# Optimization experiments

Measured on AMD Instinct MI355X. Metric: run time of the kernel, lower is better.

The kernel has to match this reference:

```python
import jax, jax.numpy as jnp
import numpy as np

B, L, H, E, D = 2, 2048, 8, 64, 64


def setup_inputs() -> dict:
    key = jax.random.key(0)
    k0, k1, k2, k3 = jax.random.split(key, 4)
    u = jax.random.normal(k0, (B, L, H, D), dtype=jnp.float32)
    q = jax.random.normal(k1, (B, L, H, E), dtype=jnp.float32)
    k = jax.random.normal(k2, (B, L, H, E), dtype=jnp.float32)
    v = jax.random.normal(k3, (B, L, H, D), dtype=jnp.float32)
    # causal mask: True where attention is DISALLOWED (strict upper triangle)
    attn_mask = jnp.triu(jnp.ones((L, L), dtype=bool), k=1)[None, None]  # (1,1,L,L)
    return {"u": u, "q": q, "k": k, "v": v, "attn_mask": attn_mask}


def reference(u, q, k, v, attn_mask):
    # q,k: [B,L,H,E]; v,u: [B,L,H,D]; attn_mask: [1,1,L,S] bool (True = masked)
    Edim = q.shape[-1]
    S = k.shape[1]
    scale = 1.0 / np.sqrt(Edim)
    scores = jnp.einsum('blhe,bshe->bhls', q, k)  # [B,H,L,S]
    x = jax.nn.relu(scale * scores)
    # attention_normalize(method='squared_relu'): relu(x)^2 / seq_len; masked -> 0
    A = jnp.where(attn_mask, 0.0, x * x) / S  # [B,H,L,S]
    # dropout is identity in eval mode
    V = u * jnp.einsum('bhls,bshd->blhd', A, v)  # [B,L,H,D]
    return V
```

## Files before the change

kernel.cpp:

```cpp
#include <hip/hip_runtime.h>
#include <hip/hip_bf16.h>

namespace {
constexpr int Lc = 2048, Hc = 8;
constexpr int RS = Hc * 64;
constexpr int NKT = 32;
constexpr int TILE_BYTES = 16384;
}

typedef __attribute__((ext_vector_type(8))) short bf16x8;
typedef __attribute__((ext_vector_type(16))) float f32x16;
typedef unsigned int u32;
typedef __attribute__((ext_vector_type(4))) u32 u32x4;

__device__ __forceinline__ u32 bfu(float x) {
    return (u32)__builtin_bit_cast(unsigned short, __float2bfloat16(x));
}
__device__ __forceinline__ short f2bf(float x) {
    return (short)__builtin_bit_cast(unsigned short, __float2bfloat16(x));
}

#define MFMA32(a, b, c) __builtin_amdgcn_mfma_f32_32x32x16_bf16((a), (b), (c), 0, 0, 0)

#define GLL16(gp, lp) __builtin_amdgcn_global_load_lds( \
    (const __attribute__((address_space(1))) unsigned int*)(gp), \
    (__attribute__((address_space(3))) unsigned int*)(lp), 16, 0, 0)

__global__ __launch_bounds__(256)
void prep_kv(const float* __restrict__ kg, const float* __restrict__ vg,
             short* __restrict__ ws)
{
    const int kt = blockIdx.x, bh = blockIdx.y;
    const int b = bh >> 3, h = bh & 7;
    const size_t base = ((size_t)b * Lc * Hc + h) * 64;
    char* tile = (char*)ws + (size_t)(bh * NKT + kt) * TILE_BYTES;
    const int tid = threadIdx.x;

    {
        const int c = tid & 7, e0 = c * 8;
        #pragma unroll
        for (int p = 0; p < 2; ++p) {
            const int s = (tid >> 3) + 32 * p;
            const float* src = kg + base + (size_t)(kt * 64 + s) * RS + e0;
            float4 x0 = *(const float4*)src;
            float4 x1 = *(const float4*)(src + 4);
            bf16x8 w = { f2bf(x0.x), f2bf(x0.y), f2bf(x0.z), f2bf(x0.w),
                         f2bf(x1.x), f2bf(x1.y), f2bf(x1.z), f2bf(x1.w) };
            const int lane = (c & 1) * 32 + (s & 31);
            const int byte = ((s >> 5) * 4 + (c >> 1)) * 1024 + lane * 16;
            *(bf16x8*)(tile + byte) = w;
        }
    }
    {
        const int d = tid & 63;
        #pragma unroll
        for (int p = 0; p < 2; ++p) {
            const int sblk = (tid >> 6) + 4 * p;
            const int s0 = sblk * 8;
            float xv[8];
            #pragma unroll
            for (int j = 0; j < 8; ++j)
                xv[j] = vg[base + (size_t)(kt * 64 + s0 + j) * RS + d];
            bf16x8 w = { f2bf(xv[0]), f2bf(xv[1]), f2bf(xv[2]), f2bf(xv[3]),
                         f2bf(xv[4]), f2bf(xv[5]), f2bf(xv[6]), f2bf(xv[7]) };
            const int lane = (sblk & 1) * 32 + (d & 31);
            const int byte = 8192 + ((d >> 5) * 4 + (sblk >> 1)) * 1024 + lane * 16;
            *(bf16x8*)(tile + byte) = w;
        }
    }
}

__global__ __launch_bounds__(512, 1)
void gate_attn(const float* __restrict__ ug, const float* __restrict__ qg,
               const short* __restrict__ ws, float* __restrict__ outg)
{
    __shared__ __align__(16) char lds[2][4 * TILE_BYTES];

    const int tid = threadIdx.x;
    const int wave = tid >> 6, lane = tid & 63;
    const int col = lane & 31, hi = lane >> 5;
    const int qs = wave & 1, ktp = wave >> 1;

    const int pr = blockIdx.x, bh = blockIdx.y;
    const int b = bh >> 3, h = bh & 7;
    const size_t base = ((size_t)b * Lc * Hc + h) * 64;
    const char* wsbh = (const char*)ws + (size_t)bh * NKT * TILE_BYTES;

    auto STAGEG = [&](int t0, int buf) {
        const char* src = wsbh + (size_t)t0 * TILE_BYTES + tid * 16;
        char* dst = &lds[buf][0] + tid * 16;
        #pragma unroll
        for (int i = 0; i < 8; ++i)
            GLL16(src + i * 8192, dst + i * 8192);
    };

    auto RUN_STRIP = [&](int strip) {
        const int NTs = strip + 1;
        const int IT = (NTs + 3) >> 2;
        const int qw = strip * 64 + qs * 32;
        const int qg_l = qw + col;

        bf16x8 qf[4];
        #pragma unroll
        for (int es = 0; es < 4; ++es) {
            const float* p = qg + base + (size_t)(qw + col) * RS + es * 16 + hi * 8;
            float4 a = *(const float4*)p;
            float4 c2 = *(const float4*)(p + 4);
            qf[es] = (bf16x8){ f2bf(a.x),  f2bf(a.y),  f2bf(a.z),  f2bf(a.w),
                               f2bf(c2.x), f2bf(c2.y), f2bf(c2.z), f2bf(c2.w) };
        }

        f32x16 oacc[2];
        #pragma unroll
        for (int r = 0; r < 16; ++r) { oacc[0][r] = 0.f; oacc[1][r] = 0.f; }

        STAGEG(0, 0);
        __syncthreads();

        for (int it = 0; it < IT; ++it) {
            if (it + 1 < IT) STAGEG(4 * (it + 1), (it & 1) ^ 1);
            const int kt = 4 * it + ktp;
            if (kt <= strip) {
                const char* kb = &lds[it & 1][0] + ktp * TILE_BYTES;

                f32x16 sacc[2];
                #pragma unroll
                for (int r = 0; r < 16; ++r) { sacc[0][r] = 0.f; sacc[1][r] = 0.f; }
                #pragma unroll
                for (int sb = 0; sb < 2; ++sb)
                    #pragma unroll
                    for (int es = 0; es < 4; ++es) {
                        bf16x8 kf = *(const bf16x8*)(kb + (sb * 4 + es) * 1024 + lane * 16);
                        sacc[sb] = MFMA32(kf, qf[es], sacc[sb]);
                    }

                const bool dmask = (kt == strip);
                u32 pa[4][4];
                #pragma unroll
                for (int sb = 0; sb < 2; ++sb) {
                    float pv[16];
                    #pragma unroll
                    for (int r = 0; r < 16; ++r) {
                        float x = sacc[sb][r];
                        x = (x > 0.f) ? x * x : 0.f;
                        const int s_g = kt * 64 + sb * 32 + (r & 3) + 8 * (r >> 2) + 4 * hi;
                        if (dmask && s_g > qg_l) x = 0.f;
                        pv[r] = x;
                    }
                    u32 W[8];
                    #pragma unroll
                    for (int t = 0; t < 8; ++t)
                        W[t] = bfu(pv[2 * t]) | (bfu(pv[2 * t + 1]) << 16);
                    asm volatile("v_permlane32_swap_b32 %0, %1" : "+v"(W[0]), "+v"(W[2]));
                    asm volatile("v_permlane32_swap_b32 %0, %1" : "+v"(W[1]), "+v"(W[3]));
                    asm volatile("v_permlane32_swap_b32 %0, %1" : "+v"(W[4]), "+v"(W[6]));
                    asm volatile("v_permlane32_swap_b32 %0, %1" : "+v"(W[5]), "+v"(W[7]));
                    pa[sb * 2 + 0][0] = W[0]; pa[sb * 2 + 0][1] = W[1];
                    pa[sb * 2 + 0][2] = W[2]; pa[sb * 2 + 0][3] = W[3];
                    pa[sb * 2 + 1][0] = W[4]; pa[sb * 2 + 1][1] = W[5];
                    pa[sb * 2 + 1][2] = W[6]; pa[sb * 2 + 1][3] = W[7];
                }

                const char* vb = kb + 8192;
                #pragma unroll
                for (int dh = 0; dh < 2; ++dh)
                    #pragma unroll
                    for (int ks = 0; ks < 4; ++ks) {
                        bf16x8 vf = *(const bf16x8*)(vb + (dh * 4 + ks) * 1024 + lane * 16);
                        u32x4 pw = { pa[ks][0], pa[ks][1], pa[ks][2], pa[ks][3] };
                        oacc[dh] = MFMA32(__builtin_bit_cast(bf16x8, pw), vf, oacc[dh]);
                    }
            }
            __syncthreads();
        }

        float* red = (float*)&lds[0][0];
        #pragma unroll
        for (int dh = 0; dh < 2; ++dh)
            #pragma unroll
            for (int r = 0; r < 16; ++r) {
                const int m = (r & 3) + 8 * (r >> 2) + 4 * hi;
                red[(((ktp * 2 + qs) * 32) + m) * 64 + dh * 32 + col] = oacc[dh][r];
            }
        __syncthreads();

        const float sc = 1.0f / (64.0f * 2048.0f);
        #pragma unroll
        for (int rr = 0; rr < 2; ++rr) {
            const int e4 = rr * 512 + tid;
            const int row = e4 >> 4, d4 = (e4 & 15) * 4;
            const int rqs = row >> 5, m = row & 31;
            float4 s = make_float4(0.f, 0.f, 0.f, 0.f);
            #pragma unroll
            for (int k = 0; k < 4; ++k) {
                const float4 p = *(const float4*)&red[(((k * 2 + rqs) * 32) + m) * 64 + d4];
                s.x += p.x; s.y += p.y; s.z += p.z; s.w += p.w;
            }
            const size_t idx = base + (size_t)(strip * 64 + row) * RS + d4;
            const float4 uu = *(const float4*)&ug[idx];
            float4 o;
            o.x = uu.x * s.x * sc; o.y = uu.y * s.y * sc;
            o.z = uu.z * s.z * sc; o.w = uu.w * s.w * sc;
            *(float4*)&outg[idx] = o;
        }
        __syncthreads();
    };

    RUN_STRIP(31 - pr);
    RUN_STRIP(pr);
}

extern "C" void kernel_launch(void* const* d_in, const int* in_sizes, int n_in,
                              void* d_out, int out_size, void* d_ws, size_t ws_size,
                              hipStream_t stream) {
    const float* u = (const float*)d_in[0];
    const float* q = (const float*)d_in[1];
    const float* k = (const float*)d_in[2];
    const float* v = (const float*)d_in[3];
    float* out = (float*)d_out;

    prep_kv<<<dim3(NKT, 16), dim3(256), 0, stream>>>(k, v, (short*)d_ws);
    gate_attn<<<dim3(16, 16), dim3(512), 0, stream>>>(u, q, (const short*)d_ws, out);
}
```

Measured before the change: 38.84 us.

## Halve waves per block, each wave covering both query halves with V from global

The attention block drops from 8 waves to 4. Each wave now computes both 32-row query halves against its key tile, so each K fragment read from LDS feeds two MFMAs. Only K tiles are staged into LDS, skipping tiles beyond the causal limit. V fragments are loaded straight from global memory into registers. This halves LDS staging traffic and shared memory use, at the cost of fewer waves per CU, more registers per wave, and global-load latency on the V path.

```diff
diff --git a/kernel.cpp b/kernel.cpp
--- a/kernel.cpp
+++ b/kernel.cpp
@@ -70,105 +70,120 @@
     }
 }
 
-__global__ __launch_bounds__(512, 1)
+__global__ __launch_bounds__(256, 1)
 void gate_attn(const float* __restrict__ ug, const float* __restrict__ qg,
                const short* __restrict__ ws, float* __restrict__ outg)
 {
-    __shared__ __align__(16) char lds[2][4 * TILE_BYTES];
+    __shared__ __align__(16) char lds[2][4 * 8192];
 
     const int tid = threadIdx.x;
-    const int wave = tid >> 6, lane = tid & 63;
+    const int ktp = tid >> 6, lane = tid & 63;
     const int col = lane & 31, hi = lane >> 5;
-    const int qs = wave & 1, ktp = wave >> 1;
 
     const int pr = blockIdx.x, bh = blockIdx.y;
     const int b = bh >> 3, h = bh & 7;
     const size_t base = ((size_t)b * Lc * Hc + h) * 64;
     const char* wsbh = (const char*)ws + (size_t)bh * NKT * TILE_BYTES;
 
-    auto STAGEG = [&](int t0, int buf) {
-        const char* src = wsbh + (size_t)t0 * TILE_BYTES + tid * 16;
-        char* dst = &lds[buf][0] + tid * 16;
-        #pragma unroll
-        for (int i = 0; i < 8; ++i)
-            GLL16(src + i * 8192, dst + i * 8192);
+    auto STAGEG = [&](int t0, int buf, int smax) {
+        #pragma unroll
+        for (int t = 0; t < 4; ++t) {
+            const int kt2 = t0 + t;
+            if (kt2 <= smax) {
+                const char* src = wsbh + (size_t)kt2 * TILE_BYTES + tid * 16;
+                char* dst = &lds[buf][t * 8192] + tid * 16;
+                GLL16(src, dst);
+                GLL16(src + 4096, dst + 4096);
+            }
+        }
     };
 
     auto RUN_STRIP = [&](int strip) {
-        const int NTs = strip + 1;
-        const int IT = (NTs + 3) >> 2;
-        const int qw = strip * 64 + qs * 32;
-        const int qg_l = qw + col;
-
-        bf16x8 qf[4];
-        #pragma unroll
-        for (int es = 0; es < 4; ++es) {
-            const float* p = qg + base + (size_t)(qw + col) * RS + es * 16 + hi * 8;
-            float4 a = *(const float4*)p;
-            float4 c2 = *(const float4*)(p + 4);
-            qf[es] = (bf16x8){ f2bf(a.x),  f2bf(a.y),  f2bf(a.z),  f2bf(a.w),
-                               f2bf(c2.x), f2bf(c2.y), f2bf(c2.z), f2bf(c2.w) };
-        }
-
-        f32x16 oacc[2];
-        #pragma unroll
-        for (int r = 0; r < 16; ++r) { oacc[0][r] = 0.f; oacc[1][r] = 0.f; }
-
-        STAGEG(0, 0);
+        const int IT = (strip + 4) >> 2;
+
+        bf16x8 qf[2][4];
+        #pragma unroll
+        for (int q2 = 0; q2 < 2; ++q2)
+            #pragma unroll
+            for (int es = 0; es < 4; ++es) {
+                const float* p = qg + base +
+                    (size_t)(strip * 64 + q2 * 32 + col) * RS + es * 16 + hi * 8;
+                float4 a = *(const float4*)p;
+                float4 c2 = *(const float4*)(p + 4);
+                qf[q2][es] = (bf16x8){ f2bf(a.x),  f2bf(a.y),  f2bf(a.z),  f2bf(a.w),
+                                       f2bf(c2.x), f2bf(c2.y), f2bf(c2.z), f2bf(c2.w) };
+            }
+
+        f32x16 oacc[2][2];
+        #pragma unroll
+        for (int q2 = 0; q2 < 2; ++q2)
+            #pragma unroll
+            for (int r = 0; r < 16; ++r) { oacc[q2][0][r] = 0.f; oacc[q2][1][r] = 0.f; }
+
+        STAGEG(0, 0, strip);
         __syncthreads();
 
         for (int it = 0; it < IT; ++it) {
-            if (it + 1 < IT) STAGEG(4 * (it + 1), (it & 1) ^ 1);
+            if (it + 1 < IT) STAGEG(4 * (it + 1), (it & 1) ^ 1, strip);
             const int kt = 4 * it + ktp;
             if (kt <= strip) {
-                const char* kb = &lds[it & 1][0] + ktp * TILE_BYTES;
-
-                f32x16 sacc[2];
-                #pragma unroll
-                for (int r = 0; r < 16; ++r) { sacc[0][r] = 0.f; sacc[1][r] = 0.f; }
-                #pragma unroll
-                for (int sb = 0; sb < 2; ++sb)
+                const char* vsrc = wsbh + (size_t)kt * TILE_BYTES + 8192 + lane * 16;
+                bf16x8 vf[2][4];
+                #pragma unroll
+                for (int dh = 0; dh < 2; ++dh)
+                    #pragma unroll
+                    for (int ks = 0; ks < 4; ++ks)
+                        vf[dh][ks] = *(const bf16x8*)(vsrc + (dh * 4 + ks) * 1024);
+
+                const char* kb = &lds[it & 1][ktp * 8192];
+                const bool dmask = (kt == strip);
+                u32 pa[2][4][4];
+
+                #pragma unroll
+                for (int sb = 0; sb < 2; ++sb) {
+                    f32x16 sacc0 = (f32x16)(0.f), sacc1 = (f32x16)(0.f);
                     #pragma unroll
                     for (int es = 0; es < 4; ++es) {
                         bf16x8 kf = *(const bf16x8*)(kb + (sb * 4 + es) * 1024 + lane * 16);
-                        sacc[sb] = MFMA32(kf, qf[es], sacc[sb]);
+                        sacc0 = MFMA32(kf, qf[0][es], sacc0);
+                        sacc1 = MFMA32(kf, qf[1][es], sacc1);
                     }
-
-                const bool dmask = (kt == strip);
-                u32 pa[4][4];
-                #pragma unroll
-                for (int sb = 0; sb < 2; ++sb) {
-                    float pv[16];
-                    #pragma unroll
-                    for (int r = 0; r < 16; ++r) {
-                        float x = sacc[sb][r];
-                        x = (x > 0.f) ? x * x : 0.f;
-                        const int s_g = kt * 64 + sb * 32 + (r & 3) + 8 * (r >> 2) + 4 * hi;
-                        if (dmask && s_g > qg_l) x = 0.f;
-                        pv[r] = x;
+                    #pragma unroll
+                    for (int q2 = 0; q2 < 2; ++q2) {
+                        const f32x16& sv = q2 ? sacc1 : sacc0;
+                        const int qg2 = strip * 64 + q2 * 32 + col;
+                        float pv[16];
+                        #pragma unroll
+                        for (int r = 0; r < 16; ++r) {
+                            float x = sv[r];
+                            x = (x > 0.f) ? x * x : 0.f;
+                            const int s_g = kt * 64 + sb * 32 + (r & 3) + 8 * (r >> 2) + 4 * hi;
+                            if (dmask && s_g > qg2) x = 0.f;
+                            pv[r] = x;
+                        }
+                        u32 W[8];
+                        #pragma unroll
+                        for (int t = 0; t < 8; ++t)
+                            W[t] = bfu(pv[2 * t]) | (bfu(pv[2 * t + 1]) << 16);
+                        asm volatile("v_permlane32_swap_b32 %0, %1" : "+v"(W[0]), "+v"(W[2]));
+                        asm volatile("v_permlane32_swap_b32 %0, %1" : "+v"(W[1]), "+v"(W[3]));
+                        asm volatile("v_permlane32_swap_b32 %0, %1" : "+v"(W[4]), "+v"(W[6]));
+                        asm volatile("v_permlane32_swap_b32 %0, %1" : "+v"(W[5]), "+v"(W[7]));
+                        pa[q2][sb * 2 + 0][0] = W[0]; pa[q2][sb * 2 + 0][1] = W[1];
+                        pa[q2][sb * 2 + 0][2] = W[2]; pa[q2][sb * 2 + 0][3] = W[3];
+                        pa[q2][sb * 2 + 1][0] = W[4]; pa[q2][sb * 2 + 1][1] = W[5];
+                        pa[q2][sb * 2 + 1][2] = W[6]; pa[q2][sb * 2 + 1][3] = W[7];
                     }
-                    u32 W[8];
-                    #pragma unroll
-                    for (int t = 0; t < 8; ++t)
-                        W[t] = bfu(pv[2 * t]) | (bfu(pv[2 * t + 1]) << 16);
-                    asm volatile("v_permlane32_swap_b32 %0, %1" : "+v"(W[0]), "+v"(W[2]));
-                    asm volatile("v_permlane32_swap_b32 %0, %1" : "+v"(W[1]), "+v"(W[3]));
-                    asm volatile("v_permlane32_swap_b32 %0, %1" : "+v"(W[4]), "+v"(W[6]));
-                    asm volatile("v_permlane32_swap_b32 %0, %1" : "+v"(W[5]), "+v"(W[7]));
-                    pa[sb * 2 + 0][0] = W[0]; pa[sb * 2 + 0][1] = W[1];
-                    pa[sb * 2 + 0][2] = W[2]; pa[sb * 2 + 0][3] = W[3];
-                    pa[sb * 2 + 1][0] = W[4]; pa[sb * 2 + 1][1] = W[5];
-                    pa[sb * 2 + 1][2] = W[6]; pa[sb * 2 + 1][3] = W[7];
                 }
 
-                const char* vb = kb + 8192;
                 #pragma unroll
                 for (int dh = 0; dh < 2; ++dh)
                     #pragma unroll
                     for (int ks = 0; ks < 4; ++ks) {
-                        bf16x8 vf = *(const bf16x8*)(vb + (dh * 4 + ks) * 1024 + lane * 16);
-                        u32x4 pw = { pa[ks][0], pa[ks][1], pa[ks][2], pa[ks][3] };
-                        oacc[dh] = MFMA32(__builtin_bit_cast(bf16x8, pw), vf, oacc[dh]);
+                        u32x4 p0 = { pa[0][ks][0], pa[0][ks][1], pa[0][ks][2], pa[0][ks][3] };
+                        u32x4 p1 = { pa[1][ks][0], pa[1][ks][1], pa[1][ks][2], pa[1][ks][3] };
+                        oacc[0][dh] = MFMA32(__builtin_bit_cast(bf16x8, p0), vf[dh][ks], oacc[0][dh]);
+                        oacc[1][dh] = MFMA32(__builtin_bit_cast(bf16x8, p1), vf[dh][ks], oacc[1][dh]);
                     }
             }
             __syncthreads();
@@ -176,27 +191,28 @@
 
         float* red = (float*)&lds[0][0];
         #pragma unroll
-        for (int dh = 0; dh < 2; ++dh)
-            #pragma unroll
-            for (int r = 0; r < 16; ++r) {
-                const int m = (r & 3) + 8 * (r >> 2) + 4 * hi;
-                red[(((ktp * 2 + qs) * 32) + m) * 64 + dh * 32 + col] = oacc[dh][r];
-            }
+        for (int q2 = 0; q2 < 2; ++q2)
+            #pragma unroll
+            for (int dh = 0; dh < 2; ++dh)
+                #pragma unroll
+                for (int r = 0; r < 16; ++r) {
+                    const int m = q2 * 32 + (r & 3) + 8 * (r >> 2) + 4 * hi;
+                    red[(ktp * 64 + m) * 64 + dh * 32 + col] = oacc[q2][dh][r];
+                }
         __syncthreads();
 
         const float sc = 1.0f / (64.0f * 2048.0f);
         #pragma unroll
-        for (int rr = 0; rr < 2; ++rr) {
-            const int e4 = rr * 512 + tid;
-            const int row = e4 >> 4, d4 = (e4 & 15) * 4;
-            const int rqs = row >> 5, m = row & 31;
+        for (int j = 0; j < 4; ++j) {
+            const int e = tid + 256 * j;
+            const int row = e >> 4, c4 = (e & 15) * 4;
             float4 s = make_float4(0.f, 0.f, 0.f, 0.f);
             #pragma unroll
             for (int k = 0; k < 4; ++k) {
-                const float4 p = *(const float4*)&red[(((k * 2 + rqs) * 32) + m) * 64 + d4];
+                const float4 p = *(const float4*)&red[(k * 64 + row) * 64 + c4];
                 s.x += p.x; s.y += p.y; s.z += p.z; s.w += p.w;
             }
-            const size_t idx = base + (size_t)(strip * 64 + row) * RS + d4;
+            const size_t idx = base + (size_t)(strip * 64 + row) * RS + c4;
             const float4 uu = *(const float4*)&ug[idx];
             float4 o;
             o.x = uu.x * s.x * sc; o.y = uu.y * s.y * sc;
@@ -220,5 +236,5 @@
     float* out = (float*)d_out;
 
     prep_kv<<<dim3(NKT, 16), dim3(256), 0, stream>>>(k, v, (short*)d_ws);
-    gate_attn<<<dim3(16, 16), dim3(512), 0, stream>>>(u, q, (const short*)d_ws, out);
-}
+    gate_attn<<<dim3(16, 16), dim3(256), 0, stream>>>(u, q, (const short*)d_ws, out);
+}
```

Result: slower. 41.81 us (+7.6%).
